# Kernel optimization log

Hardware: AMD Instinct MI355X
Metric: run time of the kernel (lower is better)

Reference implementation:

```python
import jax, jax.numpy as jnp
from jax import lax
import numpy as np

NUM_HEADS = 8
KW = 3  # window kernel size

def _avgpool3(x):
    # x: [B,C,H,W]; AvgPool2d(3,1,1) with count_include_pad=True -> sum/9
    s = lax.reduce_window(x, 0.0, lax.add, (1, 1, KW, KW), (1, 1, 1, 1),
                          ((0, 0), (0, 0), (1, 1), (1, 1)))
    return s / (KW * KW)

def _unfold3(y):
    # y: [B,h,w,C] -> [B,h,w,9,C]; patch index ordered row-major (kh,kw)
    B, h, w, C = y.shape
    yp = jnp.pad(y, ((0, 0), (1, 1), (1, 1), (0, 0)))
    return jnp.stack([yp[:, i:i + h, j:j + w, :]
                      for i in range(KW) for j in range(KW)], axis=3)

def setup_inputs():
    key = jax.random.key(0)
    ks = jax.random.split(key, 9)
    B, C, H, W = 8, 256, 64, 64
    sd = 0.02
    return {
        "x": jax.random.normal(ks[0], (B, C, H, W), jnp.float32),
        "W_qkv": jax.random.normal(ks[1], (4 * C, C), jnp.float32) * sd,
        "b_qkv": jnp.zeros((4 * C,), jnp.float32),
        "W1": jax.random.normal(ks[2], (C // 2, C), jnp.float32) * sd,
        "b1": jnp.zeros((C // 2,), jnp.float32),
        "W2": jax.random.normal(ks[3], (C, C // 2), jnp.float32) * sd,
        "b2": jnp.zeros((C,), jnp.float32),
        "Wp": jax.random.normal(ks[4], (C, C), jnp.float32) * sd,
        "bp": jnp.zeros((C,), jnp.float32),
    }

def reference(x, W_qkv, b_qkv, W1, b1, W2, b2, Wp, bp):
    B, C, H, W = x.shape
    nH = NUM_HEADS
    hd = C // nH
    scale = hd ** -0.5
    # avg pool (stride 1 keeps spatial dims), to channels-last
    y = _avgpool3(x).transpose(0, 2, 3, 1)                 # [B,h,w,C]
    qkv = y @ W_qkv.T + b_qkv                              # [B,h,w,4C]
    qkv = qkv.reshape(B, H, W, C, 4)
    q, k, v, chans = qkv[..., 0], qkv[..., 1], qkv[..., 2], qkv[..., 3]
    # channel gate
    g = jax.nn.sigmoid(jax.nn.relu(chans @ W1.T + b1) @ W2.T + b2)  # [B,h,w,C]
    # local window attention: each query attends to its 3x3 neighborhood
    qh = q.reshape(B, H, W, nH, hd)                        # [B,h,w,n,d]
    kp = _unfold3(k).reshape(B, H, W, KW * KW, nH, hd)     # [B,h,w,9,n,d]
    vp = _unfold3(v).reshape(B, H, W, KW * KW, nH, hd)
    attn = jnp.einsum('bhwnd,bhwknd->bhwnk', qh, kp) * scale
    attn = jax.nn.softmax(attn, axis=-1)
    out = jnp.einsum('bhwnk,bhwknd->bhwnd', attn, vp).reshape(B, H, W, C)
    out = out * g + out
    out = out @ Wp.T + bp
    return out.transpose(0, 3, 1, 2)                       # [B,C,H,W]
```

## Files before the change

### kernel.cpp

```cpp
#include <hip/hip_runtime.h>
#include <stdint.h>

typedef __bf16    bf16x8 __attribute__((ext_vector_type(8)));
typedef float     f32x4  __attribute__((ext_vector_type(4)));
typedef uint32_t  u32x4  __attribute__((ext_vector_type(4)));
typedef uint32_t  u32x2  __attribute__((ext_vector_type(2)));

#define MFMA(a,b,c) __builtin_amdgcn_mfma_f32_16x16x32_bf16((a),(b),(c),0,0,0)

__device__ __align__(16) uint16_t g_y [8*64*64*256];
__device__ __align__(16) uint16_t g_wpk[393216];

#define WQF 0
#define WKF 65536
#define WVF 131072
#define WCF 196608
#define W1F 262144
#define W2F 294912
#define WPF 327680

static __device__ __forceinline__ float b2f(uint32_t u){ return __builtin_bit_cast(float, u<<16); }
static __device__ __forceinline__ uint32_t f2b(float f){
  uint32_t x = __builtin_bit_cast(uint32_t, f);
  return (x + 0x7fffu + ((x>>16)&1u)) >> 16;
}

__global__ __launch_bounds__(512) void kprep(const float* __restrict__ x,
    const float* __restrict__ Wqkv, const float* __restrict__ W1,
    const float* __restrict__ W2, const float* __restrict__ Wp){
  int t = threadIdx.x;
  int bid = blockIdx.x;
  if (bid < 1024){
    __shared__ __align__(16) uint16_t sm[3*128*82];
    uint32_t* smw = (uint32_t*)sm;
    int b = bid >> 7, h = (bid >> 1) & 63, ch = (bid & 1) << 7;
    for (int i=t; i<384; i+=512){
      int base = i*41;
      smw[base+3]  = 0;
      smw[base+36] = 0;
    }
    if (h==0 || h==63){
      int hh = (h==0) ? 0 : 2;
      for (int i=t; i<5248; i+=512) smw[hh*5248 + i] = 0;
    }
    #pragma unroll
    for (int i=0;i<12;i++){
      int id = t + 512*i;
      int w4 = id&15, c = (id>>4)&127, hh = id>>11;
      int gy = h - 1 + hh;
      if ((unsigned)gy < 64u){
        f32x4 ld = *(const f32x4*)&x[(((b*256+ch+c)*64+gy)*64) + w4*4];
        int wb = (((hh*128+c)*82 + 8 + w4*4) >> 1);
        smw[wb+0] = f2b(ld[0]) | (f2b(ld[1])<<16);
        smw[wb+1] = f2b(ld[2]) | (f2b(ld[3])<<16);
      }
    }
    __syncthreads();
    int c = t & 127, wsel = t >> 7;
    int r0 = c*82, r1 = r0 + 128*82, r2 = r1 + 128*82;
    int w0 = wsel*16;
    float csp = b2f(sm[r0+w0+7]) + b2f(sm[r1+w0+7]) + b2f(sm[r2+w0+7]);
    float csc = b2f(sm[r0+w0+8]) + b2f(sm[r1+w0+8]) + b2f(sm[r2+w0+8]);
    uint16_t* dst = g_y + ((b*64+h)*64)*256 + ch + c;
    for (int j2=0;j2<16;j2++){
      int w = w0 + j2;
      float csn = b2f(sm[r0+w+9]) + b2f(sm[r1+w+9]) + b2f(sm[r2+w+9]);
      float yv = (csp + csc + csn) * (1.0f/9.0f);
      dst[w*256] = (uint16_t)f2b(yv);
      csp = csc; csc = csn;
    }
  } else {
    int idx = (bid - 1024)*512 + t;
    int j = idx & 7, lane = (idx>>3)&63;
    int n16 = lane & 15, q4 = lane>>4;
    float v;
    if (idx < 262144){
      int tt = idx >> 16, l = idx & 65535;
      int s = (l>>9)&7, nt = l>>12;
      v = Wqkv[(4*(nt*16+n16) + tt)*256 + s*32 + q4*8 + j];
    } else if (idx < 294912){
      int l = idx - 262144;
      int s = (l>>9)&7, nt = l>>12;
      v = W1[(nt*16+n16)*256 + s*32 + q4*8 + j];
    } else if (idx < 327680){
      int l = idx - 294912;
      int s = (l>>9)&3, nt = l>>11;
      v = W2[(nt*16+n16)*128 + s*32 + q4*8 + j];
    } else {
      int l = idx - 327680;
      int s = (l>>9)&7, nt = l>>12;
      v = Wp[(nt*16+n16)*256 + s*32 + q4*8 + j];
    }
    g_wpk[idx] = (uint16_t)f2b(v);
  }
}

#define YSTR  264
#define HSTR  136
#define K2_QS 15840
#define K2_KS 20192
#define K2_VS 28352
#define MCH   0
#define MHS   8448
#define MAO   15840
#define MAOSTR 266
#define MAOT  15840
#define MTSTR 36
__global__ __launch_bounds__(512,4) void kattn(const float* __restrict__ bqkv,
    const float* __restrict__ b1, const float* __restrict__ b2v,
    const float* __restrict__ bp, float* __restrict__ out){
  __shared__ __align__(16) uint16_t sm[36512];
  int t = threadIdx.x;
  int lane = t & 63, wave = t >> 6;
  int n16 = lane & 15, quad = lane >> 4;
  int bid = blockIdx.x;
  int L = (bid & 7)*128 + (bid >> 3);
  int bb = L >> 7, ty = (L >> 3) & 15, tx = L & 7;

  uint32_t opk[2][8];
  uint32_t chp[16];

  #pragma unroll
  for (int i=0;i<4;i++){
    int id = t + 512*i;
    if (id < 1920){
      int hp = id >> 5, c8 = id & 31;
      int py = hp/10, px = hp - py*10;
      int gy = ty*4 + py - 1, gx = tx*8 + px - 1;
      u32x4 ld = {0,0,0,0};
      if ((unsigned)gy<64u && (unsigned)gx<64u)
        ld = *(const u32x4*)&g_y[((bb*64+gy)*64+gx)*256 + c8*8];
      *(u32x4*)&sm[hp*YSTR + c8*8] = ld;
    }
  }
  __syncthreads();

  #pragma unroll
  for (int hf=0; hf<2; hf++){
    {
      int ntg = hf*8 + wave;
      bf16x8 Bq[8];
      #pragma unroll
      for (int s=0;s<8;s++) Bq[s] = *(const bf16x8*)&g_wpk[WQF + ((ntg*8+s)*64+lane)*8];
      float bq = bqkv[4*(ntg*16+n16) + 0];
      int colB = wave*16;
      #pragma unroll
      for (int mt=0; mt<2; mt++){
        f32x4 a = {0.f,0.f,0.f,0.f};
        int m = mt*16 + n16;
        int hrow = 10*(m>>3) + (m&7) + 11;
        #pragma unroll
        for (int s=0;s<8;s++){
          bf16x8 A = *(const bf16x8*)&sm[hrow*YSTR + s*32 + quad*8];
          a = MFMA(A, Bq[s], a);
        }
        #pragma unroll
        for (int r=0;r<4;r++){
          int row = mt*16 + quad*4 + r;
          sm[K2_QS + row*HSTR + colB + n16] = (uint16_t)f2b(a[r] + bq);
        }
      }
    }
    {
      int ntg = hf*8 + wave;
      bf16x8 Bk[8], Bv[8];
      #pragma unroll
      for (int s=0;s<8;s++){
        Bk[s] = *(const bf16x8*)&g_wpk[WKF + ((ntg*8+s)*64+lane)*8];
        Bv[s] = *(const bf16x8*)&g_wpk[WVF + ((ntg*8+s)*64+lane)*8];
      }
      float bk = bqkv[4*(ntg*16+n16) + 1];
      float bv = bqkv[4*(ntg*16+n16) + 2];
      int colB = wave*16;
      #pragma unroll
      for (int mt=0; mt<4; mt++){
        f32x4 ak = {0.f,0.f,0.f,0.f}, av = {0.f,0.f,0.f,0.f};
        int m = mt*16 + n16;
        int mr = (m < 60) ? m : 59;
        #pragma unroll
        for (int s=0;s<8;s++){
          bf16x8 A = *(const bf16x8*)&sm[mr*YSTR + s*32 + quad*8];
          ak = MFMA(A, Bk[s], ak);
          av = MFMA(A, Bv[s], av);
        }
        #pragma unroll
        for (int r=0;r<4;r++){
          int row = mt*16 + quad*4 + r;
          if (row < 60){
            int py = row/10, px = row - py*10;
            int gy = ty*4 + py - 1, gx = tx*8 + px - 1;
            bool ok = ((unsigned)gy<64u) && ((unsigned)gx<64u);
            float vk = ok ? ak[r] + bk : 0.f;
            float vv = ok ? av[r] + bv : 0.f;
            sm[K2_KS + row*HSTR + colB + n16] = (uint16_t)f2b(vk);
            sm[K2_VS + row*HSTR + colB + n16] = (uint16_t)f2b(vv);
          }
        }
      }
    }
    __syncthreads();
    if (wave < 4){
      int p = lane & 31, half = lane >> 5;
      int cb = wave*32 + half*16;
      const uint16_t* qp = &sm[K2_QS + p*HSTR + cb];
      u32x4 qa = *(const u32x4*)qp;
      u32x4 qb = *(const u32x4*)(qp+8);
      float qv[16];
      #pragma unroll
      for (int i=0;i<4;i++){
        qv[2*i]    = b2f(qa[i]&0xffffu); qv[2*i+1]   = b2f(qa[i]>>16);
        qv[8+2*i]  = b2f(qb[i]&0xffffu); qv[8+2*i+1] = b2f(qb[i]>>16);
      }
      int hb = 10*(p>>3) + (p&7) + 11;
      const int off[9] = {-11,-10,-9,-1,0,1,9,10,11};
      float sc[9];
      #pragma unroll
      for (int nb=0;nb<9;nb++){
        const uint16_t* kp = &sm[K2_KS + (hb+off[nb])*HSTR + cb];
        u32x4 ka = *(const u32x4*)kp;
        u32x4 kb = *(const u32x4*)(kp+8);
        float s = 0.f;
        #pragma unroll
        for (int i=0;i<4;i++){
          s += qv[2*i]*b2f(ka[i]&0xffffu)   + qv[2*i+1]*b2f(ka[i]>>16);
          s += qv[8+2*i]*b2f(kb[i]&0xffffu) + qv[8+2*i+1]*b2f(kb[i]>>16);
        }
        s += __shfl_xor(s, 32);
        sc[nb] = s * 0.17677669529663687f;
      }
      float mx = sc[0];
      #pragma unroll
      for (int nb=1;nb<9;nb++) mx = fmaxf(mx, sc[nb]);
      float l = 0.f;
      #pragma unroll
      for (int nb=0;nb<9;nb++){ sc[nb] = __expf(sc[nb]-mx); l += sc[nb]; }
      float inv = 1.f / l;
      float o[16];
      #pragma unroll
      for (int i=0;i<16;i++) o[i]=0.f;
      #pragma unroll
      for (int nb=0;nb<9;nb++){
        float wgt = sc[nb]*inv;
        const uint16_t* vp = &sm[K2_VS + (hb+off[nb])*HSTR + cb];
        u32x4 va = *(const u32x4*)vp;
        u32x4 vb = *(const u32x4*)(vp+8);
        #pragma unroll
        for (int i=0;i<4;i++){
          o[2*i]    += wgt*b2f(va[i]&0xffffu); o[2*i+1]   += wgt*b2f(va[i]>>16);
          o[8+2*i]  += wgt*b2f(vb[i]&0xffffu); o[8+2*i+1] += wgt*b2f(vb[i]>>16);
        }
      }
      #pragma unroll
      for (int i=0;i<8;i++) opk[hf][i] = f2b(o[2*i]) | (f2b(o[2*i+1])<<16);
    } else if (hf == 0){
      #pragma unroll
      for (int jj=0;jj<4;jj++){
        int ntg = (wave-4)*4 + jj;
        bf16x8 Bc[8];
        #pragma unroll
        for (int s=0;s<8;s++) Bc[s] = *(const bf16x8*)&g_wpk[WCF + ((ntg*8+s)*64+lane)*8];
        float bc = bqkv[4*(ntg*16+n16) + 3];
        #pragma unroll
        for (int mt=0; mt<2; mt++){
          f32x4 a = {0.f,0.f,0.f,0.f};
          int m = mt*16 + n16;
          int hrow = 10*(m>>3) + (m&7) + 11;
          #pragma unroll
          for (int s=0;s<8;s++){
            bf16x8 A = *(const bf16x8*)&sm[hrow*YSTR + s*32 + quad*8];
            a = MFMA(A, Bc[s], a);
          }
          chp[(jj*2+mt)*2+0] = f2b(a[0]+bc) | (f2b(a[1]+bc)<<16);
          chp[(jj*2+mt)*2+1] = f2b(a[2]+bc) | (f2b(a[3]+bc)<<16);
        }
      }
    } else {
      #pragma unroll
      for (int jj=0;jj<4;jj++){
        int ntg = (wave-4)*4 + jj;
        int col = ntg*16 + n16;
        #pragma unroll
        for (int mt=0;mt<2;mt++){
          #pragma unroll
          for (int r2=0;r2<2;r2++){
            uint32_t v = chp[(jj*2+mt)*2+r2];
            int row = mt*16 + quad*4 + r2*2;
            sm[MCH + row*264 + col]     = (uint16_t)(v & 0xffffu);
            sm[MCH + (row+1)*264 + col] = (uint16_t)(v >> 16);
          }
        }
      }
    }
    __syncthreads();
  }
  if (wave < 4){
    int p = lane & 31, half = lane >> 5;
    int cb = wave*32 + half*16;
    #pragma unroll
    for (int hf=0;hf<2;hf++)
      #pragma unroll
      for (int i=0;i<8;i++)
        *(uint32_t*)&sm[MAO + p*MAOSTR + hf*128 + cb + 2*i] = opk[hf][i];
  }
  {
    int ntg = wave;
    bf16x8 Bf[8];
    #pragma unroll
    for (int s=0;s<8;s++) Bf[s] = *(const bf16x8*)&g_wpk[W1F + ((ntg*8+s)*64+lane)*8];
    float bs = b1[ntg*16+n16];
    int colB = wave*16;
    #pragma unroll
    for (int mt=0;mt<2;mt++){
      f32x4 a = {0.f,0.f,0.f,0.f};
      #pragma unroll
      for (int s=0;s<8;s++){
        bf16x8 A = *(const bf16x8*)&sm[MCH + (mt*16+n16)*264 + s*32 + quad*8];
        a = MFMA(A, Bf[s], a);
      }
      #pragma unroll
      for (int r=0;r<4;r++){
        int row = mt*16 + quad*4 + r;
        sm[MHS + row*HSTR + colB + n16] = (uint16_t)f2b(fmaxf(a[r]+bs, 0.f));
      }
    }
  }
  __syncthreads();
  #pragma unroll
  for (int jj=0;jj<2;jj++){
    int ntg = wave*2 + jj;
    bf16x8 Bf[4];
    #pragma unroll
    for (int s=0;s<4;s++) Bf[s] = *(const bf16x8*)&g_wpk[W2F + ((ntg*4+s)*64+lane)*8];
    float bs = b2v[ntg*16+n16];
    int colB = ntg*16;
    #pragma unroll
    for (int mt=0;mt<2;mt++){
      f32x4 a = {0.f,0.f,0.f,0.f};
      #pragma unroll
      for (int s=0;s<4;s++){
        bf16x8 A = *(const bf16x8*)&sm[MHS + (mt*16+n16)*HSTR + s*32 + quad*8];
        a = MFMA(A, Bf[s], a);
      }
      #pragma unroll
      for (int r=0;r<4;r++){
        int row = mt*16 + quad*4 + r;
        float gg = 1.f/(1.f+__expf(-(a[r] + bs)));
        float ao = b2f((uint32_t)sm[MAO + row*MAOSTR + colB + n16]);
        sm[MCH + row*264 + colB + n16] = (uint16_t)f2b(ao*(1.f+gg));
      }
    }
  }
  __syncthreads();
  #pragma unroll
  for (int jj=0;jj<2;jj++){
    int ntg = wave*2 + jj;
    bf16x8 Bf[8];
    #pragma unroll
    for (int s=0;s<8;s++) Bf[s] = *(const bf16x8*)&g_wpk[WPF + ((ntg*8+s)*64+lane)*8];
    float bs = bp[ntg*16+n16];
    int colB = ntg*16;
    #pragma unroll
    for (int mt=0;mt<2;mt++){
      f32x4 a = {0.f,0.f,0.f,0.f};
      #pragma unroll
      for (int s=0;s<8;s++){
        bf16x8 A = *(const bf16x8*)&sm[MCH + (mt*16+n16)*264 + s*32 + quad*8];
        a = MFMA(A, Bf[s], a);
      }
      uint32_t lo = f2b(a[0]+bs) | (f2b(a[1]+bs)<<16);
      uint32_t hi = f2b(a[2]+bs) | (f2b(a[3]+bs)<<16);
      int col = colB + n16, row0 = mt*16 + quad*4;
      u32x2 pk = {lo, hi};
      *(u32x2*)&sm[MAOT + col*MTSTR + row0] = pk;
    }
  }
  __syncthreads();
  #pragma unroll
  for (int i=0;i<4;i++){
    int idx = t + 512*i;
    int ix4 = idx&1, iy = (idx>>1)&3, c = idx>>3;
    int p0 = iy*8 + ix4*4;
    u32x2 pk = *(const u32x2*)&sm[MAOT + c*MTSTR + p0];
    f32x4 stv;
    stv[0] = b2f(pk[0]&0xffffu); stv[1] = b2f(pk[0]>>16);
    stv[2] = b2f(pk[1]&0xffffu); stv[3] = b2f(pk[1]>>16);
    *(f32x4*)&out[(((bb*256+c)*64) + ty*4+iy)*64 + tx*8 + ix4*4] = stv;
  }
}

extern "C" void kernel_launch(void* const* d_in, const int* in_sizes, int n_in,
                              void* d_out, int out_size, void* d_ws, size_t ws_size,
                              hipStream_t stream){
  (void)in_sizes; (void)n_in; (void)d_ws; (void)ws_size; (void)out_size;
  const float* x    = (const float*)d_in[0];
  const float* Wqkv = (const float*)d_in[1];
  const float* bqkv = (const float*)d_in[2];
  const float* b1   = (const float*)d_in[4];
  const float* W1   = (const float*)d_in[3];
  const float* W2   = (const float*)d_in[5];
  const float* b2   = (const float*)d_in[6];
  const float* Wp   = (const float*)d_in[7];
  const float* bp   = (const float*)d_in[8];
  kprep<<<dim3(1792), dim3(512), 0, stream>>>(x, Wqkv, W1, W2, Wp);
  kattn<<<dim3(1024), dim3(512), 0, stream>>>(bqkv, b1, b2, bp, (float*)d_out);
}
```

Before: 179.6 us.

## Halve spatial tile to 2x8 pixels, doubling blocks and raising occupancy

Shrinks each attention block's tile from 4x8 to 2x8 output pixels, so the grid grows to 2048 blocks. Shared memory per block drops and launch bounds go from 4 to 6 blocks per CU. The attention work is split across more lanes (8 channels per lane with an extra shuffle reduction). The cost is more halo overhead: 40 K/V rows computed per 16 queries instead of 60 per 32. Every block also reloads all the packed weights, so total weight traffic and redundant MFMA work per output pixel both rise.

```diff
diff --git a/kernel.cpp b/kernel.cpp
--- a/kernel.cpp
+++ b/kernel.cpp
@@ -97,36 +97,35 @@
 
 #define YSTR  264
 #define HSTR  136
-#define K2_QS 15840
-#define K2_KS 20192
-#define K2_VS 28352
+#define K2_QS 10560
+#define K2_KS 12736
+#define K2_VS 18176
 #define MCH   0
-#define MHS   8448
-#define MAO   15840
+#define MHS   4224
+#define MAO   10560
 #define MAOSTR 266
-#define MAOT  15840
-#define MTSTR 36
-__global__ __launch_bounds__(512,4) void kattn(const float* __restrict__ bqkv,
+#define MAOT  10560
+#define MTSTR 20
+__global__ __launch_bounds__(512,6) void kattn(const float* __restrict__ bqkv,
     const float* __restrict__ b1, const float* __restrict__ b2v,
     const float* __restrict__ bp, float* __restrict__ out){
-  __shared__ __align__(16) uint16_t sm[36512];
+  __shared__ __align__(16) uint16_t sm[23616];
   int t = threadIdx.x;
   int lane = t & 63, wave = t >> 6;
   int n16 = lane & 15, quad = lane >> 4;
   int bid = blockIdx.x;
-  int L = (bid & 7)*128 + (bid >> 3);
-  int bb = L >> 7, ty = (L >> 3) & 15, tx = L & 7;
-
-  uint32_t opk[2][8];
-  uint32_t chp[16];
-
-  #pragma unroll
-  for (int i=0;i<4;i++){
+  int bb = bid >> 8, ty = (bid >> 3) & 31, tx = bid & 7;
+
+  uint32_t opk[2][4];
+  uint32_t chp[8];
+
+  #pragma unroll
+  for (int i=0;i<3;i++){
     int id = t + 512*i;
-    if (id < 1920){
+    if (id < 1280){
       int hp = id >> 5, c8 = id & 31;
       int py = hp/10, px = hp - py*10;
-      int gy = ty*4 + py - 1, gx = tx*8 + px - 1;
+      int gy = ty*2 + py - 1, gx = tx*8 + px - 1;
       u32x4 ld = {0,0,0,0};
       if ((unsigned)gy<64u && (unsigned)gx<64u)
         ld = *(const u32x4*)&g_y[((bb*64+gy)*64+gx)*256 + c8*8];
@@ -144,23 +143,20 @@
       for (int s=0;s<8;s++) Bq[s] = *(const bf16x8*)&g_wpk[WQF + ((ntg*8+s)*64+lane)*8];
       float bq = bqkv[4*(ntg*16+n16) + 0];
       int colB = wave*16;
-      #pragma unroll
-      for (int mt=0; mt<2; mt++){
-        f32x4 a = {0.f,0.f,0.f,0.f};
-        int m = mt*16 + n16;
-        int hrow = 10*(m>>3) + (m&7) + 11;
-        #pragma unroll
-        for (int s=0;s<8;s++){
-          bf16x8 A = *(const bf16x8*)&sm[hrow*YSTR + s*32 + quad*8];
-          a = MFMA(A, Bq[s], a);
-        }
-        #pragma unroll
-        for (int r=0;r<4;r++){
-          int row = mt*16 + quad*4 + r;
-          sm[K2_QS + row*HSTR + colB + n16] = (uint16_t)f2b(a[r] + bq);
-        }
-      }
-    }
+      f32x4 a = {0.f,0.f,0.f,0.f};
+      int hrow = 10*(n16>>3) + (n16&7) + 11;
+      #pragma unroll
+      for (int s=0;s<8;s++){
+        bf16x8 A = *(const bf16x8*)&sm[hrow*YSTR + s*32 + quad*8];
+        a = MFMA(A, Bq[s], a);
+      }
+      #pragma unroll
+      for (int r=0;r<4;r++){
+        int row = quad*4 + r;
+        sm[K2_QS + row*HSTR + colB + n16] = (uint16_t)f2b(a[r] + bq);
+      }
+    }
+    __syncthreads();
     {
       int ntg = hf*8 + wave;
       bf16x8 Bk[8], Bv[8];
@@ -173,10 +169,10 @@
       float bv = bqkv[4*(ntg*16+n16) + 2];
       int colB = wave*16;
       #pragma unroll
-      for (int mt=0; mt<4; mt++){
+      for (int mt=0; mt<3; mt++){
         f32x4 ak = {0.f,0.f,0.f,0.f}, av = {0.f,0.f,0.f,0.f};
         int m = mt*16 + n16;
-        int mr = (m < 60) ? m : 59;
+        int mr = (m < 40) ? m : 39;
         #pragma unroll
         for (int s=0;s<8;s++){
           bf16x8 A = *(const bf16x8*)&sm[mr*YSTR + s*32 + quad*8];
@@ -186,9 +182,9 @@
         #pragma unroll
         for (int r=0;r<4;r++){
           int row = mt*16 + quad*4 + r;
-          if (row < 60){
+          if (row < 40){
             int py = row/10, px = row - py*10;
-            int gy = ty*4 + py - 1, gx = tx*8 + px - 1;
+            int gy = ty*2 + py - 1, gx = tx*8 + px - 1;
             bool ok = ((unsigned)gy<64u) && ((unsigned)gx<64u);
             float vk = ok ? ak[r] + bk : 0.f;
             float vv = ok ? av[r] + bv : 0.f;
@@ -200,17 +196,13 @@
     }
     __syncthreads();
     if (wave < 4){
-      int p = lane & 31, half = lane >> 5;
-      int cb = wave*32 + half*16;
+      int p = lane & 15, part = lane >> 4;
+      int cb = wave*32 + part*8;
       const uint16_t* qp = &sm[K2_QS + p*HSTR + cb];
       u32x4 qa = *(const u32x4*)qp;
-      u32x4 qb = *(const u32x4*)(qp+8);
-      float qv[16];
-      #pragma unroll
-      for (int i=0;i<4;i++){
-        qv[2*i]    = b2f(qa[i]&0xffffu); qv[2*i+1]   = b2f(qa[i]>>16);
-        qv[8+2*i]  = b2f(qb[i]&0xffffu); qv[8+2*i+1] = b2f(qb[i]>>16);
-      }
+      float qv[8];
+      #pragma unroll
+      for (int i=0;i<4;i++){ qv[2*i]=b2f(qa[i]&0xffffu); qv[2*i+1]=b2f(qa[i]>>16); }
       int hb = 10*(p>>3) + (p&7) + 11;
       const int off[9] = {-11,-10,-9,-1,0,1,9,10,11};
       float sc[9];
@@ -218,13 +210,12 @@
       for (int nb=0;nb<9;nb++){
         const uint16_t* kp = &sm[K2_KS + (hb+off[nb])*HSTR + cb];
         u32x4 ka = *(const u32x4*)kp;
-        u32x4 kb = *(const u32x4*)(kp+8);
         float s = 0.f;
         #pragma unroll
         for (int i=0;i<4;i++){
-          s += qv[2*i]*b2f(ka[i]&0xffffu)   + qv[2*i+1]*b2f(ka[i]>>16);
-          s += qv[8+2*i]*b2f(kb[i]&0xffffu) + qv[8+2*i+1]*b2f(kb[i]>>16);
-        }
+          s += qv[2*i]*b2f(ka[i]&0xffffu) + qv[2*i+1]*b2f(ka[i]>>16);
+        }
+        s += __shfl_xor(s, 16);
         s += __shfl_xor(s, 32);
         sc[nb] = s * 0.17677669529663687f;
       }
@@ -235,23 +226,21 @@
       #pragma unroll
       for (int nb=0;nb<9;nb++){ sc[nb] = __expf(sc[nb]-mx); l += sc[nb]; }
       float inv = 1.f / l;
-      float o[16];
-      #pragma unroll
-      for (int i=0;i<16;i++) o[i]=0.f;
+      float o[8];
+      #pragma unroll
+      for (int i=0;i<8;i++) o[i]=0.f;
       #pragma unroll
       for (int nb=0;nb<9;nb++){
         float wgt = sc[nb]*inv;
         const uint16_t* vp = &sm[K2_VS + (hb+off[nb])*HSTR + cb];
         u32x4 va = *(const u32x4*)vp;
-        u32x4 vb = *(const u32x4*)(vp+8);
         #pragma unroll
         for (int i=0;i<4;i++){
-          o[2*i]    += wgt*b2f(va[i]&0xffffu); o[2*i+1]   += wgt*b2f(va[i]>>16);
-          o[8+2*i]  += wgt*b2f(vb[i]&0xffffu); o[8+2*i+1] += wgt*b2f(vb[i]>>16);
-        }
-      }
-      #pragma unroll
-      for (int i=0;i<8;i++) opk[hf][i] = f2b(o[2*i]) | (f2b(o[2*i+1])<<16);
+          o[2*i] += wgt*b2f(va[i]&0xffffu); o[2*i+1] += wgt*b2f(va[i]>>16);
+        }
+      }
+      #pragma unroll
+      for (int i=0;i<4;i++) opk[hf][i] = f2b(o[2*i]) | (f2b(o[2*i+1])<<16);
     } else if (hf == 0){
       #pragma unroll
       for (int jj=0;jj<4;jj++){
@@ -260,19 +249,15 @@
         #pragma unroll
         for (int s=0;s<8;s++) Bc[s] = *(const bf16x8*)&g_wpk[WCF + ((ntg*8+s)*64+lane)*8];
         float bc = bqkv[4*(ntg*16+n16) + 3];
-        #pragma unroll
-        for (int mt=0; mt<2; mt++){
-          f32x4 a = {0.f,0.f,0.f,0.f};
-          int m = mt*16 + n16;
-          int hrow = 10*(m>>3) + (m&7) + 11;
-          #pragma unroll
-          for (int s=0;s<8;s++){
-            bf16x8 A = *(const bf16x8*)&sm[hrow*YSTR + s*32 + quad*8];
-            a = MFMA(A, Bc[s], a);
-          }
-          chp[(jj*2+mt)*2+0] = f2b(a[0]+bc) | (f2b(a[1]+bc)<<16);
-          chp[(jj*2+mt)*2+1] = f2b(a[2]+bc) | (f2b(a[3]+bc)<<16);
-        }
+        f32x4 a = {0.f,0.f,0.f,0.f};
+        int hrow = 10*(n16>>3) + (n16&7) + 11;
+        #pragma unroll
+        for (int s=0;s<8;s++){
+          bf16x8 A = *(const bf16x8*)&sm[hrow*YSTR + s*32 + quad*8];
+          a = MFMA(A, Bc[s], a);
+        }
+        chp[jj*2+0] = f2b(a[0]+bc) | (f2b(a[1]+bc)<<16);
+        chp[jj*2+1] = f2b(a[2]+bc) | (f2b(a[3]+bc)<<16);
       }
     } else {
       #pragma unroll
@@ -280,26 +265,23 @@
         int ntg = (wave-4)*4 + jj;
         int col = ntg*16 + n16;
         #pragma unroll
-        for (int mt=0;mt<2;mt++){
-          #pragma unroll
-          for (int r2=0;r2<2;r2++){
-            uint32_t v = chp[(jj*2+mt)*2+r2];
-            int row = mt*16 + quad*4 + r2*2;
-            sm[MCH + row*264 + col]     = (uint16_t)(v & 0xffffu);
-            sm[MCH + (row+1)*264 + col] = (uint16_t)(v >> 16);
-          }
+        for (int r2=0;r2<2;r2++){
+          uint32_t v = chp[jj*2+r2];
+          int row = quad*4 + r2*2;
+          sm[MCH + row*264 + col]     = (uint16_t)(v & 0xffffu);
+          sm[MCH + (row+1)*264 + col] = (uint16_t)(v >> 16);
         }
       }
     }
     __syncthreads();
   }
   if (wave < 4){
-    int p = lane & 31, half = lane >> 5;
-    int cb = wave*32 + half*16;
+    int p = lane & 15, part = lane >> 4;
+    int cb = wave*32 + part*8;
     #pragma unroll
     for (int hf=0;hf<2;hf++)
       #pragma unroll
-      for (int i=0;i<8;i++)
+      for (int i=0;i<4;i++)
         *(uint32_t*)&sm[MAO + p*MAOSTR + hf*128 + cb + 2*i] = opk[hf][i];
   }
   {
@@ -309,19 +291,16 @@
     for (int s=0;s<8;s++) Bf[s] = *(const bf16x8*)&g_wpk[W1F + ((ntg*8+s)*64+lane)*8];
     float bs = b1[ntg*16+n16];
     int colB = wave*16;
-    #pragma unroll
-    for (int mt=0;mt<2;mt++){
-      f32x4 a = {0.f,0.f,0.f,0.f};
-      #pragma unroll
-      for (int s=0;s<8;s++){
-        bf16x8 A = *(const bf16x8*)&sm[MCH + (mt*16+n16)*264 + s*32 + quad*8];
-        a = MFMA(A, Bf[s], a);
-      }
-      #pragma unroll
-      for (int r=0;r<4;r++){
-        int row = mt*16 + quad*4 + r;
-        sm[MHS + row*HSTR + colB + n16] = (uint16_t)f2b(fmaxf(a[r]+bs, 0.f));
-      }
+    f32x4 a = {0.f,0.f,0.f,0.f};
+    #pragma unroll
+    for (int s=0;s<8;s++){
+      bf16x8 A = *(const bf16x8*)&sm[MCH + n16*264 + s*32 + quad*8];
+      a = MFMA(A, Bf[s], a);
+    }
+    #pragma unroll
+    for (int r=0;r<4;r++){
+      int row = quad*4 + r;
+      sm[MHS + row*HSTR + colB + n16] = (uint16_t)f2b(fmaxf(a[r]+bs, 0.f));
     }
   }
   __syncthreads();
@@ -333,21 +312,18 @@
     for (int s=0;s<4;s++) Bf[s] = *(const bf16x8*)&g_wpk[W2F + ((ntg*4+s)*64+lane)*8];
     float bs = b2v[ntg*16+n16];
     int colB = ntg*16;
-    #pragma unroll
-    for (int mt=0;mt<2;mt++){
-      f32x4 a = {0.f,0.f,0.f,0.f};
-      #pragma unroll
-      for (int s=0;s<4;s++){
-        bf16x8 A = *(const bf16x8*)&sm[MHS + (mt*16+n16)*HSTR + s*32 + quad*8];
-        a = MFMA(A, Bf[s], a);
-      }
-      #pragma unroll
-      for (int r=0;r<4;r++){
-        int row = mt*16 + quad*4 + r;
-        float gg = 1.f/(1.f+__expf(-(a[r] + bs)));
-        float ao = b2f((uint32_t)sm[MAO + row*MAOSTR + colB + n16]);
-        sm[MCH + row*264 + colB + n16] = (uint16_t)f2b(ao*(1.f+gg));
-      }
+    f32x4 a = {0.f,0.f,0.f,0.f};
+    #pragma unroll
+    for (int s=0;s<4;s++){
+      bf16x8 A = *(const bf16x8*)&sm[MHS + n16*HSTR + s*32 + quad*8];
+      a = MFMA(A, Bf[s], a);
+    }
+    #pragma unroll
+    for (int r=0;r<4;r++){
+      int row = quad*4 + r;
+      float gg = 1.f/(1.f+__expf(-(a[r] + bs)));
+      float ao = b2f((uint32_t)sm[MAO + row*MAOSTR + colB + n16]);
+      sm[MCH + row*264 + colB + n16] = (uint16_t)f2b(ao*(1.f+gg));
     }
   }
   __syncthreads();
@@ -359,32 +335,29 @@
     for (int s=0;s<8;s++) Bf[s] = *(const bf16x8*)&g_wpk[WPF + ((ntg*8+s)*64+lane)*8];
     float bs = bp[ntg*16+n16];
     int colB = ntg*16;
-    #pragma unroll
-    for (int mt=0;mt<2;mt++){
-      f32x4 a = {0.f,0.f,0.f,0.f};
-      #pragma unroll
-      for (int s=0;s<8;s++){
-        bf16x8 A = *(const bf16x8*)&sm[MCH + (mt*16+n16)*264 + s*32 + quad*8];
-        a = MFMA(A, Bf[s], a);
-      }
-      uint32_t lo = f2b(a[0]+bs) | (f2b(a[1]+bs)<<16);
-      uint32_t hi = f2b(a[2]+bs) | (f2b(a[3]+bs)<<16);
-      int col = colB + n16, row0 = mt*16 + quad*4;
-      u32x2 pk = {lo, hi};
-      *(u32x2*)&sm[MAOT + col*MTSTR + row0] = pk;
-    }
+    f32x4 a = {0.f,0.f,0.f,0.f};
+    #pragma unroll
+    for (int s=0;s<8;s++){
+      bf16x8 A = *(const bf16x8*)&sm[MCH + n16*264 + s*32 + quad*8];
+      a = MFMA(A, Bf[s], a);
+    }
+    uint32_t lo = f2b(a[0]+bs) | (f2b(a[1]+bs)<<16);
+    uint32_t hi = f2b(a[2]+bs) | (f2b(a[3]+bs)<<16);
+    int col = colB + n16, row0 = quad*4;
+    u32x2 pk = {lo, hi};
+    *(u32x2*)&sm[MAOT + col*MTSTR + row0] = pk;
   }
   __syncthreads();
   #pragma unroll
-  for (int i=0;i<4;i++){
+  for (int i=0;i<2;i++){
     int idx = t + 512*i;
-    int ix4 = idx&1, iy = (idx>>1)&3, c = idx>>3;
+    int ix4 = idx&1, iy = (idx>>1)&1, c = idx>>2;
     int p0 = iy*8 + ix4*4;
     u32x2 pk = *(const u32x2*)&sm[MAOT + c*MTSTR + p0];
     f32x4 stv;
     stv[0] = b2f(pk[0]&0xffffu); stv[1] = b2f(pk[0]>>16);
     stv[2] = b2f(pk[1]&0xffffu); stv[3] = b2f(pk[1]>>16);
-    *(f32x4*)&out[(((bb*256+c)*64) + ty*4+iy)*64 + tx*8 + ix4*4] = stv;
+    *(f32x4*)&out[(((bb*256+c)*64) + ty*2+iy)*64 + tx*8 + ix4*4] = stv;
   }
 }
 
@@ -395,12 +368,12 @@
   const float* x    = (const float*)d_in[0];
   const float* Wqkv = (const float*)d_in[1];
   const float* bqkv = (const float*)d_in[2];
+  const float* W1   = (const float*)d_in[3];
   const float* b1   = (const float*)d_in[4];
-  const float* W1   = (const float*)d_in[3];
   const float* W2   = (const float*)d_in[5];
   const float* b2   = (const float*)d_in[6];
   const float* Wp   = (const float*)d_in[7];
   const float* bp   = (const float*)d_in[8];
   kprep<<<dim3(1792), dim3(512), 0, stream>>>(x, Wqkv, W1, W2, Wp);
-  kattn<<<dim3(1024), dim3(512), 0, stream>>>(bqkv, b1, b2, bp, (float*)d_out);
+  kattn<<<dim3(2048), dim3(512), 0, stream>>>(bqkv, b1, b2, bp, (float*)d_out);
 }
```

Measured after the change: 398.5 us. 2.22x slower.
